# Kernel optimization log

Measured on AMD Instinct MI355X. Metric: run time of the kernel, lower is better.

The kernel has to match this reference:

```python
import jax, jax.numpy as jnp
import numpy as np

EMBED_DIM = 1024
NUM_HEADS = 16
HEAD_DIM = EMBED_DIM // NUM_HEADS


def setup_inputs() -> dict:
    key = jax.random.key(0)
    k_x, k_qw, k_qb, k_ow, k_ob = jax.random.split(key, 5)
    B, T, C = 4, 2048, EMBED_DIM
    s = 1.0 / np.sqrt(C)
    return {
        "x": jax.random.normal(k_x, (B, T, C), dtype=jnp.float32),
        # torch nn.Linear weights: [out_features, in_features]
        "qkv_w": jax.random.uniform(k_qw, (3 * C, C), jnp.float32, -s, s),
        "qkv_b": jax.random.uniform(k_qb, (3 * C,), jnp.float32, -s, s),
        "out_w": jax.random.uniform(k_ow, (C, C), jnp.float32, -s, s),
        "out_b": jax.random.uniform(k_ob, (C,), jnp.float32, -s, s),
    }


def reference(x, qkv_w, qkv_b, out_w, out_b):
    B, T, C = x.shape
    H, D = NUM_HEADS, HEAD_DIM
    qkv = x @ qkv_w.T + qkv_b                      # [B,T,3C]
    qkv = qkv.reshape(B, T, 3, H, D).transpose(2, 0, 3, 1, 4)  # [3,B,H,T,D]
    Q, K, V = qkv[0], qkv[1], qkv[2]
    scores = jnp.einsum("bhtd,bhsd->bhts", Q, K) / np.sqrt(D).astype(np.float32)
    causal = jnp.triu(jnp.ones((T, T), dtype=bool), k=1)        # mask future
    scores = jnp.where(causal, -jnp.inf, scores)
    attn_weights = jax.nn.softmax(scores, axis=-1)              # [B,H,T,T]
    out = jnp.einsum("bhts,bhsd->bhtd", attn_weights, V)
    out = out.transpose(0, 2, 1, 3).reshape(B, T, C)
    return out @ out_w.T + out_b, attn_weights
```

## Files before the change

### kernel.cpp

```cpp
#include <hip/hip_runtime.h>
#include <cstdint>
#include <cstddef>

#define Bq  4
#define Tq  2048
#define Cq  1024
#define Hq  16
#define Dq  64
#define BTq 8192
#define C3q 3072

using bf16x8 = __attribute__((ext_vector_type(8))) short;
using f32x4  = __attribute__((ext_vector_type(4))) float;
using us4    = __attribute__((ext_vector_type(4))) unsigned short;

__device__ __forceinline__ unsigned short f2bf(float f) {
  unsigned u = __builtin_bit_cast(unsigned, f);
  return (unsigned short)((u + 0x7fffu + ((u >> 16) & 1u)) >> 16);
}
__device__ __forceinline__ float bf2f(unsigned short h) {
  return __builtin_bit_cast(float, (unsigned)h << 16);
}

__device__ __forceinline__ void gload_lds16(const void* g, void* l) {
  __builtin_amdgcn_global_load_lds(
      (const __attribute__((address_space(1))) void*)g,
      (__attribute__((address_space(3))) void*)l, 16, 0, 0);
}

__global__ __launch_bounds__(256) void cvt_kernel(const float* __restrict__ src,
                                                  unsigned short* __restrict__ dst, int n4) {
  int i = blockIdx.x * 256 + threadIdx.x;
  int stride = gridDim.x * 256;
  for (; i < n4; i += stride) {
    float4 v = reinterpret_cast<const float4*>(src)[i];
    us4 o = { f2bf(v.x), f2bf(v.y), f2bf(v.z), f2bf(v.w) };
    reinterpret_cast<us4*>(dst)[i] = o;
  }
}

template<int EPI>
__global__ __launch_bounds__(256) void gemm128(
    const unsigned short* __restrict__ A, const unsigned short* __restrict__ Bw,
    const float* __restrict__ bias,
    unsigned short* __restrict__ Qb, unsigned short* __restrict__ Kb,
    unsigned short* __restrict__ Vtb, float* __restrict__ Cout,
    int M, int N, int K)
{
  __shared__ unsigned short As[128][32];
  __shared__ unsigned short Bs[128][32];
  const int n0 = blockIdx.x * 128, m0 = blockIdx.y * 128;
  const int tid = threadIdx.x;
  const int w = tid >> 6, l = tid & 63, r = l & 15, g = l >> 4;
  const int wm = w >> 1, wn = w & 1;
  const int ldRow = tid >> 2, ldCol = (tid & 3) * 8;
  f32x4 acc[4][4] = {};

  const unsigned short* Ar0 = A  + (size_t)(m0 +      ldRow) * K + ldCol;
  const unsigned short* Ar1 = A  + (size_t)(m0 + 64 + ldRow) * K + ldCol;
  const unsigned short* Br0 = Bw + (size_t)(n0 +      ldRow) * K + ldCol;
  const unsigned short* Br1 = Bw + (size_t)(n0 + 64 + ldRow) * K + ldCol;
  char* Ab0 = (char*)&As[0][0]        + w * 1024;
  char* Ab1 = (char*)&As[0][0] + 4096 + w * 1024;
  char* Bb0 = (char*)&Bs[0][0]        + w * 1024;
  char* Bb1 = (char*)&Bs[0][0] + 4096 + w * 1024;

  for (int k0 = 0; k0 < K; k0 += 32) {
    __syncthreads();
    gload_lds16(Ar0 + k0, Ab0);
    gload_lds16(Ar1 + k0, Ab1);
    gload_lds16(Br0 + k0, Bb0);
    gload_lds16(Br1 + k0, Bb1);
    __syncthreads();
    bf16x8 a[4], b[4];
    #pragma unroll
    for (int i = 0; i < 4; ++i) a[i] = *(const bf16x8*)&As[wm*64 + i*16 + r][g*8];
    #pragma unroll
    for (int j = 0; j < 4; ++j) b[j] = *(const bf16x8*)&Bs[wn*64 + j*16 + r][g*8];
    #pragma unroll
    for (int i = 0; i < 4; ++i)
      #pragma unroll
      for (int j = 0; j < 4; ++j)
        acc[i][j] = __builtin_amdgcn_mfma_f32_16x16x32_bf16(a[i], b[j], acc[i][j], 0, 0, 0);
  }

  if (EPI == 0) {
    const int which = n0 >> 10;
    #pragma unroll
    for (int i = 0; i < 4; ++i)
      #pragma unroll
      for (int j = 0; j < 4; ++j) {
        int gc  = n0 + wn*64 + j*16 + r;
        int gr0 = m0 + wm*64 + i*16 + 4*g;
        float bv = bias[gc];
        int hd = gc & 1023;
        int h = hd >> 6, d = hd & 63;
        if (which == 2) {
          int b = gr0 >> 11, t0 = gr0 & 2047;
          int bh = b*Hq + h;
          us4 pk = { f2bf(acc[i][j][0] + bv), f2bf(acc[i][j][1] + bv),
                     f2bf(acc[i][j][2] + bv), f2bf(acc[i][j][3] + bv) };
          *(us4*)&Vtb[(size_t)(bh*Dq + d)*Tq + t0] = pk;
        } else {
          unsigned short* dst = which ? Kb : Qb;
          #pragma unroll
          for (int jj = 0; jj < 4; ++jj) {
            int gr = gr0 + jj;
            int b = gr >> 11, t = gr & 2047;
            int bh = b*Hq + h;
            dst[(size_t)(bh*Tq + t)*Dq + d] = f2bf(acc[i][j][jj] + bv);
          }
        }
      }
  } else {
    #pragma unroll
    for (int i = 0; i < 4; ++i)
      #pragma unroll
      for (int j = 0; j < 4; ++j) {
        int gc = n0 + wn*64 + j*16 + r;
        float bv = bias[gc];
        #pragma unroll
        for (int jj = 0; jj < 4; ++jj) {
          int gr = m0 + wm*64 + i*16 + 4*g + jj;
          Cout[(size_t)gr * N + gc] = acc[i][j][jj] + bv;
        }
      }
  }
}

#define PROWB 4224
#define XMASK(row_) ((((row_) & 7) << 4) ^ ((((row_) >> 2) & 3) << 5))

__global__ __launch_bounds__(512, 4) void attn_kernel(
    const unsigned short* __restrict__ Qb, const unsigned short* __restrict__ Kb,
    const unsigned short* __restrict__ Vtb,
    float* __restrict__ attn, unsigned short* __restrict__ ctxb)
{
  __shared__ __align__(16) unsigned short P[16][2112];
  __shared__ float red[8][32];
  __shared__ float invl_s[32];

  const int p  = blockIdx.x;
  const int bh = blockIdx.y;
  const int tid = threadIdx.x, w = tid >> 6, l = tid & 63, r = l & 15, g = l >> 4;
  const int qbA = p * 16, qbB = (127 - p) * 16;
  const int NA = (qbA + 16 + 31) >> 5;
  const int NB = (qbB + 16 + 31) >> 5;
  const int LAc = NA * 32, LBc = NB * 32;

  const unsigned short* Qp = Qb  + (size_t)bh * Tq * Dq;
  const unsigned short* Kp = Kb  + (size_t)bh * Tq * Dq;
  const unsigned short* Vp = Vtb + (size_t)bh * Dq * Tq;
  char* Pmut = (char*)&P[0][0];

  bf16x8 aqA0 = *(const bf16x8*)&Qp[(size_t)(qbA + r)*Dq      + g*8];
  bf16x8 aqA1 = *(const bf16x8*)&Qp[(size_t)(qbA + r)*Dq + 32 + g*8];
  bf16x8 aqB0 = *(const bf16x8*)&Qp[(size_t)(qbB + r)*Dq      + g*8];
  bf16x8 aqB1 = *(const bf16x8*)&Qp[(size_t)(qbB + r)*Dq + 32 + g*8];

  float lsumA[4] = {0.f,0.f,0.f,0.f}, lsumB[4] = {0.f,0.f,0.f,0.f};

#define LOADK(ci_, D00, D01, D10, D11)                                              \
  {                                                                                 \
    int cj_ = ((ci_) < NA) ? (ci_) : (ci_) - NA;                                    \
    int k0c_ = cj_ * 32;                                                            \
    D00 = *(const bf16x8*)&Kp[(size_t)(k0c_ + r)*Dq      + g*8];                    \
    D01 = *(const bf16x8*)&Kp[(size_t)(k0c_ + r)*Dq + 32 + g*8];                    \
    D10 = *(const bf16x8*)&Kp[(size_t)(k0c_ + 16 + r)*Dq      + g*8];               \
    D11 = *(const bf16x8*)&Kp[(size_t)(k0c_ + 16 + r)*Dq + 32 + g*8];               \
  }

  {
    bf16x8 k00, k01, k10, k11, n00, n01, n10, n11;
    int ci = w;
    if (ci < 65) LOADK(ci, k00, k01, k10, k11);
    for (; ci < 65; ci += 8) {
      if (ci + 8 < 65) LOADK(ci + 8, n00, n01, n10, n11);
      const bool isA = ci < NA;
      const int cj  = isA ? ci : ci - NA;
      const int k0c = cj * 32;
      const int qb_ = isA ? qbA : qbB;
      const int cb_ = isA ? k0c : LAc + k0c;
      bf16x8 q0_ = isA ? aqA0 : aqB0;
      bf16x8 q1_ = isA ? aqA1 : aqB1;
      f32x4 z = {0.f,0.f,0.f,0.f};
      __builtin_amdgcn_s_setprio(1);
      f32x4 s0 = __builtin_amdgcn_mfma_f32_16x16x32_bf16(q0_, k00, z, 0, 0, 0);
      s0 = __builtin_amdgcn_mfma_f32_16x16x32_bf16(q1_, k01, s0, 0, 0, 0);
      f32x4 s1 = __builtin_amdgcn_mfma_f32_16x16x32_bf16(q0_, k10, z, 0, 0, 0);
      s1 = __builtin_amdgcn_mfma_f32_16x16x32_bf16(q1_, k11, s1, 0, 0, 0);
      __builtin_amdgcn_s_setprio(0);
      float tch[4];
      #pragma unroll
      for (int jj = 0; jj < 4; ++jj) {
        int q = qb_ + 4*g + jj;
        float p0 = (k0c + r      <= q) ? __expf(s0[jj]*0.125f) : 0.f;
        float p1 = (k0c + 16 + r <= q) ? __expf(s1[jj]*0.125f) : 0.f;
        tch[jj] = p0 + p1;
        int row = 4*g + jj, xm = XMASK(row);
        *(unsigned short*)(Pmut + row*PROWB + (((cb_ + r)*2)      ^ xm)) = f2bf(p0);
        *(unsigned short*)(Pmut + row*PROWB + (((cb_ + 16 + r)*2) ^ xm)) = f2bf(p1);
      }
      if (isA) { lsumA[0]+=tch[0]; lsumA[1]+=tch[1]; lsumA[2]+=tch[2]; lsumA[3]+=tch[3]; }
      else     { lsumB[0]+=tch[0]; lsumB[1]+=tch[1]; lsumB[2]+=tch[2]; lsumB[3]+=tch[3]; }
      k00 = n00; k01 = n01; k10 = n10; k11 = n11;
    }
  }

  #pragma unroll
  for (int jj = 0; jj < 4; ++jj) {
    float sa = lsumA[jj], sb = lsumB[jj];
    #pragma unroll
    for (int off = 1; off < 16; off <<= 1) {
      sa += __shfl_xor(sa, off, 64);
      sb += __shfl_xor(sb, off, 64);
    }
    if (r == 0) { red[w][4*g + jj] = sa; red[w][16 + 4*g + jj] = sb; }
  }
  __syncthreads();
  if (tid < 32) {
    float s = 0.f;
    #pragma unroll
    for (int ww = 0; ww < 8; ++ww) s += red[ww][tid];
    invl_s[tid] = 1.f / s;
  }
  __syncthreads();

  if (w < 4) {
    #pragma unroll
    for (int s = 0; s < 2; ++s) {
      const int idx   = s * 256 + tid;
      const int s16   = idx >> 8;
      const int row16 = (idx >> 4) & 15;
      const int seg   = (idx & 15) * 8;
      const int xm16  = XMASK(row16);
      const char* Prow = Pmut + row16 * PROWB;
      const int Lc    = s16 ? LBc : LAc;
      const int cbase = s16 ? LAc : 0;
      float inv = invl_s[s16*16 + row16];
      size_t ob = ((size_t)bh*Tq + (s16 ? qbB : qbA) + row16) * Tq;
      for (int cb = seg; cb < Tq; cb += 128) {
        f32x4 v0 = {0.f,0.f,0.f,0.f}, v1 = {0.f,0.f,0.f,0.f};
        if (cb < Lc) {
          bf16x8 pv = *(const bf16x8*)(Prow + (((cbase + cb)*2) ^ xm16));
          v0[0]=bf2f((unsigned short)pv[0])*inv; v0[1]=bf2f((unsigned short)pv[1])*inv;
          v0[2]=bf2f((unsigned short)pv[2])*inv; v0[3]=bf2f((unsigned short)pv[3])*inv;
          v1[0]=bf2f((unsigned short)pv[4])*inv; v1[1]=bf2f((unsigned short)pv[5])*inv;
          v1[2]=bf2f((unsigned short)pv[6])*inv; v1[3]=bf2f((unsigned short)pv[7])*inv;
        }
        __builtin_nontemporal_store(v0, (f32x4*)&attn[ob + cb]);
        __builtin_nontemporal_store(v1, (f32x4*)&attn[ob + cb + 4]);
      }
    }
  } else {
    const int dblk = w - 4;
    const char* Pr = Pmut + r * PROWB;
    const int xr = XMASK(r);
    const unsigned short* Vrow = &Vp[(size_t)(dblk*16 + r) * Tq];
    f32x4 coA0 = {0.f,0.f,0.f,0.f}, coA1 = {0.f,0.f,0.f,0.f};
    f32x4 coB0 = {0.f,0.f,0.f,0.f}, coB1 = {0.f,0.f,0.f,0.f};
    bf16x8 pa, bv, pan, bvn;
    {
      pa = *(const bf16x8*)(Pr + (((0 + g*8)*2) ^ xr));
      bv = *(const bf16x8*)&Vrow[g*8];
    }
    for (int ci = 0; ci < 65; ++ci) {
      if (ci + 1 < 65) {
        int cn = ci + 1;
        int cj = (cn < NA) ? cn : cn - NA;
        int cb = (cn < NA) ? cn*32 : LAc + cj*32;
        pan = *(const bf16x8*)(Pr + (((cb + g*8)*2) ^ xr));
        bvn = *(const bf16x8*)&Vrow[cj*32 + g*8];
      }
      if (ci < NA) {
        if (ci & 1) coA1 = __builtin_amdgcn_mfma_f32_16x16x32_bf16(pa, bv, coA1, 0, 0, 0);
        else        coA0 = __builtin_amdgcn_mfma_f32_16x16x32_bf16(pa, bv, coA0, 0, 0, 0);
      } else {
        if (ci & 1) coB1 = __builtin_amdgcn_mfma_f32_16x16x32_bf16(pa, bv, coB1, 0, 0, 0);
        else        coB0 = __builtin_amdgcn_mfma_f32_16x16x32_bf16(pa, bv, coB0, 0, 0, 0);
      }
      pa = pan; bv = bvn;
    }
    const int b = bh >> 4, h = bh & 15;
    #pragma unroll
    for (int jj = 0; jj < 4; ++jj) {
      int tA = qbA + 4*g + jj;
      ctxb[(size_t)(b*Tq + tA)*Cq + h*Dq + dblk*16 + r] =
          f2bf((coA0[jj] + coA1[jj]) * invl_s[4*g + jj]);
      int tB = qbB + 4*g + jj;
      ctxb[(size_t)(b*Tq + tB)*Cq + h*Dq + dblk*16 + r] =
          f2bf((coB0[jj] + coB1[jj]) * invl_s[16 + 4*g + jj]);
    }
  }
#undef LOADK
}

extern "C" void kernel_launch(void* const* d_in, const int* in_sizes, int n_in,
                              void* d_out, int out_size, void* d_ws, size_t ws_size,
                              hipStream_t stream) {
  const float* x     = (const float*)d_in[0];
  const float* qkv_w = (const float*)d_in[1];
  const float* qkv_b = (const float*)d_in[2];
  const float* out_w = (const float*)d_in[3];
  const float* out_b = (const float*)d_in[4];
  float* out  = (float*)d_out;
  float* attn = out + (size_t)BTq * Cq;

  char* ws = (char*)d_ws;
  unsigned short* xb    = (unsigned short*)(ws);
  unsigned short* wqkvb = (unsigned short*)(ws + (16u << 20));
  unsigned short* woutb = (unsigned short*)(ws + (22u << 20));
  unsigned short* Qb    = (unsigned short*)(ws + (24u << 20));
  unsigned short* Kb    = (unsigned short*)(ws + (40u << 20));
  unsigned short* Vtb   = (unsigned short*)(ws + (56u << 20));
  unsigned short* ctxb  = (unsigned short*)(ws + (72u << 20));

  cvt_kernel<<<2048, 256, 0, stream>>>(x,     xb,    (BTq * Cq) / 4);
  cvt_kernel<<<1024, 256, 0, stream>>>(qkv_w, wqkvb, (C3q * Cq) / 4);
  cvt_kernel<<<512,  256, 0, stream>>>(out_w, woutb, (Cq * Cq) / 4);

  dim3 g1(C3q / 128, BTq / 128);
  gemm128<0><<<g1, 256, 0, stream>>>(xb, wqkvb, qkv_b, Qb, Kb, Vtb, nullptr, BTq, C3q, Cq);

  dim3 g2(64, Bq * Hq);
  attn_kernel<<<g2, 512, 0, stream>>>(Qb, Kb, Vtb, attn, ctxb);

  dim3 g3(Cq / 128, BTq / 128);
  gemm128<1><<<g3, 256, 0, stream>>>(ctxb, woutb, out_b, nullptr, nullptr, nullptr, out, BTq, Cq, Cq);
}
```

Baseline: 504.7 us.

## Swizzle GEMM and attention block order for XCD locality; merge conversions

Adds an XCD-aware block-index swizzle with grouped tile ordering to both GEMMs, so that workgroups sharing A and B panels run on the same chiplet and reuse its L2. The attention grid is remapped the same way, keeping blocks of the same batch-head together on one XCD to share K and V. The three fp32-to-bf16 conversion launches are merged into one kernel. The cost is a few integer operations per block and a per-element branch in the conversion loop; if the grid size is not a multiple of 8 the remapping could misassign tiles, though both grids here divide evenly.

New measurement: 510.6 us. Within noise of the previous version (+1.2%).

```diff
diff --git a/kernel.cpp b/kernel.cpp
--- a/kernel.cpp
+++ b/kernel.cpp
@@ -28,14 +28,35 @@
       (__attribute__((address_space(3))) void*)l, 16, 0, 0);
 }
 
-__global__ __launch_bounds__(256) void cvt_kernel(const float* __restrict__ src,
-                                                  unsigned short* __restrict__ dst, int n4) {
+__device__ __forceinline__ void swz_tile(int gx, int gy, int& bx, int& by) {
+  const int GROUP = 8;
+  int nwg = gx * gy;
+  int raw = blockIdx.x + gx * blockIdx.y;
+  int id  = (raw & 7) * (nwg >> 3) + (raw >> 3);
+  int per = GROUP * gx;
+  int grp = id / per;
+  int rem = id - grp * per;
+  int first = grp * GROUP;
+  int gsz = (gy - first < GROUP) ? (gy - first) : GROUP;
+  by = first + rem % gsz;
+  bx = rem / gsz;
+}
+
+__global__ __launch_bounds__(256) void cvt3_kernel(
+    const float* __restrict__ s0, unsigned short* __restrict__ d0, int n0,
+    const float* __restrict__ s1, unsigned short* __restrict__ d1, int n1,
+    const float* __restrict__ s2, unsigned short* __restrict__ d2, int n2) {
   int i = blockIdx.x * 256 + threadIdx.x;
   int stride = gridDim.x * 256;
-  for (; i < n4; i += stride) {
-    float4 v = reinterpret_cast<const float4*>(src)[i];
+  int ntot = n0 + n1 + n2;
+  for (; i < ntot; i += stride) {
+    const float* src; unsigned short* dst; int j = i;
+    if (j < n0) { src = s0; dst = d0; }
+    else if ((j -= n0) < n1) { src = s1; dst = d1; }
+    else { j -= n1; src = s2; dst = d2; }
+    float4 v = reinterpret_cast<const float4*>(src)[j];
     us4 o = { f2bf(v.x), f2bf(v.y), f2bf(v.z), f2bf(v.w) };
-    reinterpret_cast<us4*>(dst)[i] = o;
+    reinterpret_cast<us4*>(dst)[j] = o;
   }
 }
 
@@ -49,7 +70,9 @@
 {
   __shared__ unsigned short As[128][32];
   __shared__ unsigned short Bs[128][32];
-  const int n0 = blockIdx.x * 128, m0 = blockIdx.y * 128;
+  int bx, by;
+  swz_tile(gridDim.x, gridDim.y, bx, by);
+  const int n0 = bx * 128, m0 = by * 128;
   const int tid = threadIdx.x;
   const int w = tid >> 6, l = tid & 63, r = l & 15, g = l >> 4;
   const int wm = w >> 1, wn = w & 1;
@@ -140,8 +163,11 @@
   __shared__ float red[8][32];
   __shared__ float invl_s[32];
 
-  const int p  = blockIdx.x;
-  const int bh = blockIdx.y;
+  const int raw = blockIdx.x + 64 * blockIdx.y;
+  const int id  = (raw & 7) * 512 + (raw >> 3);
+  const int p   = id & 63;
+  const int bh  = id >> 6;
+
   const int tid = threadIdx.x, w = tid >> 6, l = tid & 63, r = l & 15, g = l >> 4;
   const int qbA = p * 16, qbB = (127 - p) * 16;
   const int NA = (qbA + 16 + 31) >> 5;
@@ -315,9 +341,10 @@
   unsigned short* Vtb   = (unsigned short*)(ws + (56u << 20));
   unsigned short* ctxb  = (unsigned short*)(ws + (72u << 20));
 
-  cvt_kernel<<<2048, 256, 0, stream>>>(x,     xb,    (BTq * Cq) / 4);
-  cvt_kernel<<<1024, 256, 0, stream>>>(qkv_w, wqkvb, (C3q * Cq) / 4);
-  cvt_kernel<<<512,  256, 0, stream>>>(out_w, woutb, (Cq * Cq) / 4);
+  cvt3_kernel<<<2048, 256, 0, stream>>>(
+      x,     xb,    (BTq * Cq) / 4,
+      qkv_w, wqkvb, (C3q * Cq) / 4,
+      out_w, woutb, (Cq * Cq) / 4);
 
   dim3 g1(C3q / 128, BTq / 128);
   gemm128<0><<<g1, 256, 0, stream>>>(xb, wqkvb, qkv_b, Qb, Kb, Vtb, nullptr, BTq, C3q, Cq);
```

## Stage QKV epilogue through LDS for coalesced stores; transpose score MFMA operands

Applied to the files above, without the earlier changes.

The QKV GEMM epilogue now writes bias-added bf16 tiles into a shared buffer and then emits coalesced 16-byte stores to Q, K and the transposed V layout, replacing scattered 2-byte and strided writes. In the attention kernel, the K and Q operands of the score MFMA are swapped so each lane holds four consecutive key columns for one query row. This lets P be written to LDS as 8-byte vectors and cuts the row-sum reduction to two shuffles. The cost is extra barriers and an LDS transpose in the GEMM epilogue.

After: 520.7 us. 1.03x slower.

```diff
diff --git a/kernel.cpp b/kernel.cpp
--- a/kernel.cpp
+++ b/kernel.cpp
@@ -47,8 +47,9 @@
     unsigned short* __restrict__ Vtb, float* __restrict__ Cout,
     int M, int N, int K)
 {
-  __shared__ unsigned short As[128][32];
-  __shared__ unsigned short Bs[128][32];
+  __shared__ __align__(16) unsigned short S[8704];
+  unsigned short* As = S;
+  unsigned short* Bs = S + 4096;
   const int n0 = blockIdx.x * 128, m0 = blockIdx.y * 128;
   const int tid = threadIdx.x;
   const int w = tid >> 6, l = tid & 63, r = l & 15, g = l >> 4;
@@ -60,10 +61,10 @@
   const unsigned short* Ar1 = A  + (size_t)(m0 + 64 + ldRow) * K + ldCol;
   const unsigned short* Br0 = Bw + (size_t)(n0 +      ldRow) * K + ldCol;
   const unsigned short* Br1 = Bw + (size_t)(n0 + 64 + ldRow) * K + ldCol;
-  char* Ab0 = (char*)&As[0][0]        + w * 1024;
-  char* Ab1 = (char*)&As[0][0] + 4096 + w * 1024;
-  char* Bb0 = (char*)&Bs[0][0]        + w * 1024;
-  char* Bb1 = (char*)&Bs[0][0] + 4096 + w * 1024;
+  char* Ab0 = (char*)As        + w * 1024;
+  char* Ab1 = (char*)As + 4096 + w * 1024;
+  char* Bb0 = (char*)Bs        + w * 1024;
+  char* Bb1 = (char*)Bs + 4096 + w * 1024;
 
   for (int k0 = 0; k0 < K; k0 += 32) {
     __syncthreads();
@@ -74,9 +75,9 @@
     __syncthreads();
     bf16x8 a[4], b[4];
     #pragma unroll
-    for (int i = 0; i < 4; ++i) a[i] = *(const bf16x8*)&As[wm*64 + i*16 + r][g*8];
-    #pragma unroll
-    for (int j = 0; j < 4; ++j) b[j] = *(const bf16x8*)&Bs[wn*64 + j*16 + r][g*8];
+    for (int i = 0; i < 4; ++i) a[i] = *(const bf16x8*)&As[(wm*64 + i*16 + r)*32 + g*8];
+    #pragma unroll
+    for (int j = 0; j < 4; ++j) b[j] = *(const bf16x8*)&Bs[(wn*64 + j*16 + r)*32 + g*8];
     #pragma unroll
     for (int i = 0; i < 4; ++i)
       #pragma unroll
@@ -86,32 +87,50 @@
 
   if (EPI == 0) {
     const int which = n0 >> 10;
-    #pragma unroll
-    for (int i = 0; i < 4; ++i)
-      #pragma unroll
-      for (int j = 0; j < 4; ++j) {
-        int gc  = n0 + wn*64 + j*16 + r;
-        int gr0 = m0 + wm*64 + i*16 + 4*g;
-        float bv = bias[gc];
-        int hd = gc & 1023;
-        int h = hd >> 6, d = hd & 63;
-        if (which == 2) {
-          int b = gr0 >> 11, t0 = gr0 & 2047;
-          int bh = b*Hq + h;
-          us4 pk = { f2bf(acc[i][j][0] + bv), f2bf(acc[i][j][1] + bv),
-                     f2bf(acc[i][j][2] + bv), f2bf(acc[i][j][3] + bv) };
-          *(us4*)&Vtb[(size_t)(bh*Dq + d)*Tq + t0] = pk;
-        } else {
-          unsigned short* dst = which ? Kb : Qb;
+    __syncthreads();
+    #pragma unroll
+    for (int hh = 0; hh < 2; ++hh) {
+      if (hh) __syncthreads();
+      if (wn == hh) {
+        #pragma unroll
+        for (int i = 0; i < 4; ++i)
           #pragma unroll
-          for (int jj = 0; jj < 4; ++jj) {
-            int gr = gr0 + jj;
-            int b = gr >> 11, t = gr & 2047;
-            int bh = b*Hq + h;
-            dst[(size_t)(bh*Tq + t)*Dq + d] = f2bf(acc[i][j][jj] + bv);
+          for (int j = 0; j < 4; ++j) {
+            int c = j*16 + r;
+            float bv = bias[n0 + hh*64 + c];
+            int t = wm*64 + i*16 + 4*g;
+            us4 pk = { f2bf(acc[i][j][0]+bv), f2bf(acc[i][j][1]+bv),
+                       f2bf(acc[i][j][2]+bv), f2bf(acc[i][j][3]+bv) };
+            *(us4*)&S[c*136 + t] = pk;
           }
+      }
+      __syncthreads();
+      const int hd = (n0 & 1023) + hh*64;
+      const int h  = hd >> 6;
+      if (which == 2) {
+        int d = tid >> 2, tp = tid & 3;
+        int bh = (m0 >> 11)*Hq + h;
+        size_t base = ((size_t)(bh*Dq + d))*Tq + (m0 & 2047) + tp*32;
+        const unsigned short* Lr = &S[d*136 + tp*32];
+        #pragma unroll
+        for (int q4 = 0; q4 < 4; ++q4)
+          *(bf16x8*)&Vtb[base + q4*8] = *(const bf16x8*)&Lr[q4*8];
+      } else {
+        unsigned short* dst = which ? Kb : Qb;
+        int t = tid >> 1, dp = tid & 1;
+        int gr = m0 + t;
+        int bh = (gr >> 11)*Hq + h;
+        size_t base = ((size_t)(bh*Tq + (gr & 2047)))*Dq + dp*32;
+        #pragma unroll
+        for (int q4 = 0; q4 < 4; ++q4) {
+          bf16x8 vv;
+          #pragma unroll
+          for (int e = 0; e < 8; ++e)
+            vv[e] = (short)S[(dp*32 + q4*8 + e)*136 + t];
+          *(bf16x8*)&dst[base + q4*8] = vv;
         }
       }
+    }
   } else {
     #pragma unroll
     for (int i = 0; i < 4; ++i)
@@ -158,8 +177,6 @@
   bf16x8 aqB0 = *(const bf16x8*)&Qp[(size_t)(qbB + r)*Dq      + g*8];
   bf16x8 aqB1 = *(const bf16x8*)&Qp[(size_t)(qbB + r)*Dq + 32 + g*8];
 
-  float lsumA[4] = {0.f,0.f,0.f,0.f}, lsumB[4] = {0.f,0.f,0.f,0.f};
-
 #define LOADK(ci_, D00, D01, D10, D11)                                              \
   {                                                                                 \
     int cj_ = ((ci_) < NA) ? (ci_) : (ci_) - NA;                                    \
@@ -170,7 +187,9 @@
     D11 = *(const bf16x8*)&Kp[(size_t)(k0c_ + 16 + r)*Dq + 32 + g*8];               \
   }
 
+  float lsumA = 0.f, lsumB = 0.f;
   {
+    const int xm = XMASK(r);
     bf16x8 k00, k01, k10, k11, n00, n01, n10, n11;
     int ci = w;
     if (ci < 65) LOADK(ci, k00, k01, k10, k11);
@@ -179,43 +198,42 @@
       const bool isA = ci < NA;
       const int cj  = isA ? ci : ci - NA;
       const int k0c = cj * 32;
-      const int qb_ = isA ? qbA : qbB;
       const int cb_ = isA ? k0c : LAc + k0c;
       bf16x8 q0_ = isA ? aqA0 : aqB0;
       bf16x8 q1_ = isA ? aqA1 : aqB1;
+      const int q = (isA ? qbA : qbB) + r;
       f32x4 z = {0.f,0.f,0.f,0.f};
       __builtin_amdgcn_s_setprio(1);
-      f32x4 s0 = __builtin_amdgcn_mfma_f32_16x16x32_bf16(q0_, k00, z, 0, 0, 0);
-      s0 = __builtin_amdgcn_mfma_f32_16x16x32_bf16(q1_, k01, s0, 0, 0, 0);
-      f32x4 s1 = __builtin_amdgcn_mfma_f32_16x16x32_bf16(q0_, k10, z, 0, 0, 0);
-      s1 = __builtin_amdgcn_mfma_f32_16x16x32_bf16(q1_, k11, s1, 0, 0, 0);
+      f32x4 s0 = __builtin_amdgcn_mfma_f32_16x16x32_bf16(k00, q0_, z, 0, 0, 0);
+      s0 = __builtin_amdgcn_mfma_f32_16x16x32_bf16(k01, q1_, s0, 0, 0, 0);
+      f32x4 s1 = __builtin_amdgcn_mfma_f32_16x16x32_bf16(k10, q0_, z, 0, 0, 0);
+      s1 = __builtin_amdgcn_mfma_f32_16x16x32_bf16(k11, q1_, s1, 0, 0, 0);
       __builtin_amdgcn_s_setprio(0);
-      float tch[4];
-      #pragma unroll
-      for (int jj = 0; jj < 4; ++jj) {
-        int q = qb_ + 4*g + jj;
-        float p0 = (k0c + r      <= q) ? __expf(s0[jj]*0.125f) : 0.f;
-        float p1 = (k0c + 16 + r <= q) ? __expf(s1[jj]*0.125f) : 0.f;
-        tch[jj] = p0 + p1;
-        int row = 4*g + jj, xm = XMASK(row);
-        *(unsigned short*)(Pmut + row*PROWB + (((cb_ + r)*2)      ^ xm)) = f2bf(p0);
-        *(unsigned short*)(Pmut + row*PROWB + (((cb_ + 16 + r)*2) ^ xm)) = f2bf(p1);
-      }
-      if (isA) { lsumA[0]+=tch[0]; lsumA[1]+=tch[1]; lsumA[2]+=tch[2]; lsumA[3]+=tch[3]; }
-      else     { lsumB[0]+=tch[0]; lsumB[1]+=tch[1]; lsumB[2]+=tch[2]; lsumB[3]+=tch[3]; }
+      const int lim0 = q - (k0c + 4*g);
+      const int lim1 = lim0 - 16;
+      float p00 = (0 <= lim0) ? __expf(s0[0]*0.125f) : 0.f;
+      float p01 = (1 <= lim0) ? __expf(s0[1]*0.125f) : 0.f;
+      float p02 = (2 <= lim0) ? __expf(s0[2]*0.125f) : 0.f;
+      float p03 = (3 <= lim0) ? __expf(s0[3]*0.125f) : 0.f;
+      float p10 = (0 <= lim1) ? __expf(s1[0]*0.125f) : 0.f;
+      float p11 = (1 <= lim1) ? __expf(s1[1]*0.125f) : 0.f;
+      float p12 = (2 <= lim1) ? __expf(s1[2]*0.125f) : 0.f;
+      float p13 = (3 <= lim1) ? __expf(s1[3]*0.125f) : 0.f;
+      float s8 = ((p00 + p01) + (p02 + p03)) + ((p10 + p11) + (p12 + p13));
+      if (isA) lsumA += s8; else lsumB += s8;
+      us4 w0 = { f2bf(p00), f2bf(p01), f2bf(p02), f2bf(p03) };
+      us4 w1 = { f2bf(p10), f2bf(p11), f2bf(p12), f2bf(p13) };
+      *(us4*)(Pmut + r*PROWB + (((cb_ +      4*g)*2) ^ xm)) = w0;
+      *(us4*)(Pmut + r*PROWB + (((cb_ + 16 + 4*g)*2) ^ xm)) = w1;
       k00 = n00; k01 = n01; k10 = n10; k11 = n11;
     }
   }
 
-  #pragma unroll
-  for (int jj = 0; jj < 4; ++jj) {
-    float sa = lsumA[jj], sb = lsumB[jj];
-    #pragma unroll
-    for (int off = 1; off < 16; off <<= 1) {
-      sa += __shfl_xor(sa, off, 64);
-      sb += __shfl_xor(sb, off, 64);
-    }
-    if (r == 0) { red[w][4*g + jj] = sa; red[w][16 + 4*g + jj] = sb; }
+  {
+    float sa = lsumA, sb = lsumB;
+    sa += __shfl_xor(sa, 16, 64);  sa += __shfl_xor(sa, 32, 64);
+    sb += __shfl_xor(sb, 16, 64);  sb += __shfl_xor(sb, 32, 64);
+    if (l < 16) { red[w][r] = sa; red[w][16 + r] = sb; }
   }
   __syncthreads();
   if (tid < 32) {
```
